# Performance work log

Measured on AMD Instinct MI355X. Metric: run time of the kernel, lower is better.

## Reference

```python
import jax, jax.numpy as jnp
import numpy as np

M = 12          # persons per frame
K = 2           # partition channels from conv1da (1024 = 2*512)
D = 512         # GCN channel dim / LSTM hidden
C_IN = 4096     # backbone feature dim
NUM_CLASSES = 8


def setup_inputs() -> dict:
    key = jax.random.key(0)
    ks = jax.random.split(key, 8)
    N, T = 16, 32
    NT = N * T
    base_out = jax.random.normal(ks[0], (NT, M, C_IN), dtype=jnp.float32)
    dist = jax.random.uniform(ks[1], (N, T, 3, K, M, M), dtype=jnp.float32)
    # conv1da: Conv1d(4096 -> 1024, k=1, bias=False) == matmul with [1024, 4096]
    w_a = jax.random.normal(ks[2], (K * D, C_IN), dtype=jnp.float32) * 0.02
    # LSTM(512, 512, 1): torch gate order i, f, g, o
    s = 1.0 / np.sqrt(D)
    w_ih = jax.random.uniform(ks[3], (4 * D, D), minval=-s, maxval=s, dtype=jnp.float32)
    w_hh = jax.random.uniform(ks[4], (4 * D, D), minval=-s, maxval=s, dtype=jnp.float32)
    b_ih = jax.random.uniform(ks[5], (4 * D,), minval=-s, maxval=s, dtype=jnp.float32)
    b_hh = jax.random.uniform(ks[6], (4 * D,), minval=-s, maxval=s, dtype=jnp.float32)
    # gclassifier: Linear(512 -> num_classes)
    w_cls = jax.random.normal(ks[7], (NUM_CLASSES, D), dtype=jnp.float32) * 0.01
    b_cls = jnp.zeros((NUM_CLASSES,), dtype=jnp.float32)
    return {"base_out": base_out, "dist": dist, "w_a": w_a,
            "w_ih": w_ih, "w_hh": w_hh, "b_ih": b_ih, "b_hh": b_hh,
            "w_cls": w_cls, "b_cls": b_cls, "n_videos": N}


def reference(base_out, dist, w_a, w_ih, w_hh, b_ih, b_hh, w_cls, b_cls, n_videos):
    NT = base_out.shape[0]
    N = n_videos
    T = NT // N
    # conv1da (1x1 conv, no bias): [NT, M, 4096] -> [NT, K*D, M] -> [NT, K, D, M]
    node1 = jnp.einsum('nmc,oc->nom', base_out, w_a).reshape(NT, K, D, M)
    # fused three-way adjacency aggregation: node1a + node1b + node1c
    A = (dist[:, :, 2] + dist[:, :, 1] + dist[:, :, 0]).reshape(NT, K, M, M)
    node = jnp.einsum('nkcv,nkvw->ncw', node1, A)  # [NT, D, M]
    node = jax.nn.relu(node)
    # AdaptiveAvgPool1d(1) over the M persons
    pooled = node.mean(axis=2)                      # [NT, D]
    seq = pooled.reshape(N, T, D)
    # torch nn.LSTM default batch_first=False: iterates over axis 0 (N), batch=T
    def step(carry, x_t):
        h, c = carry
        g = x_t @ w_ih.T + b_ih + h @ w_hh.T + b_hh  # [T, 4D]
        i, f, gg, o = jnp.split(g, 4, axis=-1)
        c = jax.nn.sigmoid(f) * c + jax.nn.sigmoid(i) * jnp.tanh(gg)
        h = jax.nn.sigmoid(o) * jnp.tanh(c)
        return (h, c), h
    h0 = jnp.zeros((T, D), dtype=seq.dtype)
    c0 = jnp.zeros((T, D), dtype=seq.dtype)
    _, hs = jax.lax.scan(step, (h0, c0), seq)       # [N, T, D]
    last = hs[:, -1, :]                              # video_feat[:, -1, :]
    return last @ w_cls.T + b_cls                    # [N, num_classes]
```

## Files before the change

### kernel.cpp

```cpp
#include <hip/hip_runtime.h>
#include <math.h>

#define MM 12
#define KK 2
#define DD 512
#define CIN 4096
#define NCLS 8
#define NV 16
#define TT 32

typedef unsigned long long u64;
typedef __attribute__((ext_vector_type(8))) __bf16 bf16x8;
typedef __attribute__((ext_vector_type(4))) float f32x4;

#define PART_F   0
#define POOLED_F 786432
#define TAGA_F   794624
#define TAGB_F   794880
#define PART_KS_STRIDE (192 * 1024)

#define MFMA_BF16(A, B, C) __builtin_amdgcn_mfma_f32_16x16x32_bf16((A), (B), (C), 0, 0, 0)

__global__ __launch_bounds__(256, 1) void k_fused(
    const float* __restrict__ base_out, const float* __restrict__ dist,
    const float* __restrict__ w_a, const float* __restrict__ w_ih,
    const float* __restrict__ w_hh, const float* __restrict__ b_ih,
    const float* __restrict__ b_hh, const float* __restrict__ w_cls,
    const float* __restrict__ b_cls,
    float* __restrict__ part, float* __restrict__ pooled,
    unsigned* __restrict__ tagA, unsigned* __restrict__ tagB,
    u64* __restrict__ slots, float* __restrict__ out)
{
  const int wg = blockIdx.x;
  const int tid = threadIdx.x;

  __shared__ __align__(16) unsigned short Ah[16 * 40], Al[16 * 40];
  __shared__ __align__(16) unsigned short Bh[192 * 40], Bl[192 * 40];
  __shared__ __align__(16) float whh_s[16][516];
  __shared__ __align__(16) float wih_s[16][516];
  __shared__ __align__(16) float pooled_s[16][520];
  __shared__ float gx_s[16][20];
  __shared__ __align__(16) float h_s[DD];
  __shared__ float dot_s[16];
  __shared__ float Asum_s[KK * MM * MM];

  {
    const int ks = wg >> 6, ot = wg & 63;
    const int cc0 = ks * 1024;
    const int wave = tid >> 6, lane = tid & 63;
    const int jf0 = wave * 3;

    const int sq = tid & 7;
    const int sr = tid >> 3;
    unsigned boff[6];
#pragma unroll
    for (int rep = 0; rep < 6; ++rep) {
      const int j = sr + 32 * rep;
      const int n = j / 12, m = j - n * 12;
      boff[rep] = (unsigned)(((n * TT + 31) * MM + m) * CIN + cc0 + sq * 4);
    }
    const bool aact = tid < 128;
    unsigned aoff = aact ? (unsigned)((ot * 16 + (tid >> 3)) * CIN + cc0 + sq * 4) : 0u;

    f32x4 acc0 = {0.f, 0.f, 0.f, 0.f}, acc1 = acc0, acc2 = acc0;

    float4 pa, pb[6];
    if (aact) pa = *(const float4*)&w_a[aoff];
#pragma unroll
    for (int rep = 0; rep < 6; ++rep) pb[rep] = *(const float4*)&base_out[boff[rep]];

    for (int st = 0; st < 32; ++st) {
      __syncthreads();
      if (aact) {
        const int idx = (tid >> 3) * 40 + sq * 4;
        unsigned ux = __float_as_uint(pa.x), uy = __float_as_uint(pa.y);
        unsigned uz = __float_as_uint(pa.z), uw = __float_as_uint(pa.w);
        *(uint2*)&Ah[idx] = make_uint2((ux >> 16) | (uy & 0xFFFF0000u),
                                       (uz >> 16) | (uw & 0xFFFF0000u));
        unsigned lx = __float_as_uint(pa.x - __uint_as_float(ux & 0xFFFF0000u));
        unsigned ly = __float_as_uint(pa.y - __uint_as_float(uy & 0xFFFF0000u));
        unsigned lz = __float_as_uint(pa.z - __uint_as_float(uz & 0xFFFF0000u));
        unsigned lw = __float_as_uint(pa.w - __uint_as_float(uw & 0xFFFF0000u));
        *(uint2*)&Al[idx] = make_uint2((lx >> 16) | (ly & 0xFFFF0000u),
                                       (lz >> 16) | (lw & 0xFFFF0000u));
      }
#pragma unroll
      for (int rep = 0; rep < 6; ++rep) {
        const int idx = (sr + 32 * rep) * 40 + sq * 4;
        unsigned ux = __float_as_uint(pb[rep].x), uy = __float_as_uint(pb[rep].y);
        unsigned uz = __float_as_uint(pb[rep].z), uw = __float_as_uint(pb[rep].w);
        *(uint2*)&Bh[idx] = make_uint2((ux >> 16) | (uy & 0xFFFF0000u),
                                       (uz >> 16) | (uw & 0xFFFF0000u));
        unsigned lx = __float_as_uint(pb[rep].x - __uint_as_float(ux & 0xFFFF0000u));
        unsigned ly = __float_as_uint(pb[rep].y - __uint_as_float(uy & 0xFFFF0000u));
        unsigned lz = __float_as_uint(pb[rep].z - __uint_as_float(uz & 0xFFFF0000u));
        unsigned lw = __float_as_uint(pb[rep].w - __uint_as_float(uw & 0xFFFF0000u));
        *(uint2*)&Bl[idx] = make_uint2((lx >> 16) | (ly & 0xFFFF0000u),
                                       (lz >> 16) | (lw & 0xFFFF0000u));
      }
      __syncthreads();
      if (st < 31) {
        aoff += 32;
        if (aact) pa = *(const float4*)&w_a[aoff];
#pragma unroll
        for (int rep = 0; rep < 6; ++rep) {
          boff[rep] += 32;
          pb[rep] = *(const float4*)&base_out[boff[rep]];
        }
      }
      const int koff = (lane >> 4) * 8;
      const int fra = (lane & 15) * 40 + koff;
      bf16x8 oh = *(const bf16x8*)&Ah[fra];
      bf16x8 ol = *(const bf16x8*)&Al[fra];
      {
        const int r0 = ((jf0 + 0) * 16 + (lane & 15)) * 40 + koff;
        bf16x8 jh = *(const bf16x8*)&Bh[r0], jl = *(const bf16x8*)&Bl[r0];
        acc0 = MFMA_BF16(jh, oh, acc0);
        acc0 = MFMA_BF16(jh, ol, acc0);
        acc0 = MFMA_BF16(jl, oh, acc0);
      }
      {
        const int r1 = ((jf0 + 1) * 16 + (lane & 15)) * 40 + koff;
        bf16x8 jh = *(const bf16x8*)&Bh[r1], jl = *(const bf16x8*)&Bl[r1];
        acc1 = MFMA_BF16(jh, oh, acc1);
        acc1 = MFMA_BF16(jh, ol, acc1);
        acc1 = MFMA_BF16(jl, oh, acc1);
      }
      {
        const int r2 = ((jf0 + 2) * 16 + (lane & 15)) * 40 + koff;
        bf16x8 jh = *(const bf16x8*)&Bh[r2], jl = *(const bf16x8*)&Bl[r2];
        acc2 = MFMA_BF16(jh, oh, acc2);
        acc2 = MFMA_BF16(jh, ol, acc2);
        acc2 = MFMA_BF16(jl, oh, acc2);
      }
    }
    const int o = ot * 16 + (lane & 15);
    const int jr = (lane >> 4) * 4;
#pragma unroll
    for (int r = 0; r < 4; ++r) {
      part[((size_t)ks * 192 + (jf0 + 0) * 16 + jr + r) * 1024 + o] = acc0[r];
      part[((size_t)ks * 192 + (jf0 + 1) * 16 + jr + r) * 1024 + o] = acc1[r];
      part[((size_t)ks * 192 + (jf0 + 2) * 16 + jr + r) * 1024 + o] = acc2[r];
    }
    __syncthreads();
    if (tid == 0)
      __hip_atomic_store(&tagA[wg], 1u, __ATOMIC_RELEASE, __HIP_MEMORY_SCOPE_AGENT);
  }

  if (wg < 128) {
    for (int f = tid; f < 16 * DD; f += 256) {
      const int rl = f >> 9, col = f & 511;
      const int row = (rl >> 2) * DD + wg * 4 + (rl & 3);
      whh_s[rl][col] = w_hh[(size_t)row * DD + col];
      wih_s[rl][col] = w_ih[(size_t)row * DD + col];
    }
  }

  while (__hip_atomic_load(&tagA[tid], __ATOMIC_RELAXED, __HIP_MEMORY_SCOPE_AGENT) != 1u) {}
  __syncthreads();
  (void)__hip_atomic_load(&tagA[0], __ATOMIC_ACQUIRE, __HIP_MEMORY_SCOPE_AGENT);

  {
    const int n = wg >> 4, cb = (wg & 15) * 32;
    const unsigned dbase = (unsigned)((n * TT + 31) * (3 * KK * MM * MM));
    for (int f = tid; f < KK * MM * MM; f += 256)
      Asum_s[f] = dist[dbase + f] + dist[dbase + KK * MM * MM + f]
                + dist[dbase + 2 * KK * MM * MM + f];
    __syncthreads();
    if (tid < 32) {
      const int c = cb + tid;
      float nd[KK][MM];
#pragma unroll
      for (int k = 0; k < KK; ++k)
#pragma unroll
        for (int v = 0; v < MM; ++v) {
          const size_t off = (size_t)(n * MM + v) * 1024 + k * DD + c;
          nd[k][v] = part[off] + part[off + PART_KS_STRIDE]
                   + part[off + 2 * PART_KS_STRIDE] + part[off + 3 * PART_KS_STRIDE];
        }
      float accm = 0.f;
#pragma unroll
      for (int w = 0; w < MM; ++w) {
        float sw = 0.f;
#pragma unroll
        for (int k = 0; k < KK; ++k)
#pragma unroll
          for (int v = 0; v < MM; ++v) sw += nd[k][v] * Asum_s[(k * MM + v) * MM + w];
        accm += fmaxf(sw, 0.f);
      }
      pooled[n * DD + c] = accm * (1.f / 12.f);
    }
    __syncthreads();
    if (tid == 0)
      __hip_atomic_store(&tagB[wg], 1u, __ATOMIC_RELEASE, __HIP_MEMORY_SCOPE_AGENT);
  }
  if (wg >= 128) return;

  while (__hip_atomic_load(&tagB[tid], __ATOMIC_RELAXED, __HIP_MEMORY_SCOPE_AGENT) != 1u) {}
  __syncthreads();
  (void)__hip_atomic_load(&tagB[0], __ATOMIC_ACQUIRE, __HIP_MEMORY_SCOPE_AGENT);

  for (int f = tid; f < NV * DD; f += 256) pooled_s[f >> 9][f & 511] = pooled[f];
  __syncthreads();
  {
    const int rl = tid & 15, n = tid >> 4;
    const float4* wr = (const float4*)&wih_s[rl][0];
    const float4* pv = (const float4*)&pooled_s[n][0];
    float a = 0.f;
#pragma unroll 8
    for (int q = 0; q < DD / 4; ++q) {
      float4 x = wr[q], y = pv[q];
      a += x.x * y.x + x.y * y.y + x.z * y.z + x.w * y.w;
    }
    const int row = (rl >> 2) * DD + wg * 4 + (rl & 3);
    gx_s[n][rl] = a + b_ih[row] + b_hh[row];
  }
  __syncthreads();

  {
    float c_reg = 0.f;
    const int r = tid >> 4;
    const int lj = tid & 15;

    for (int s = 0; s < NV; ++s) {
      if (s == 0) {
        h_s[tid] = 0.f; h_s[tid + 256] = 0.f;
      } else {
        const u64* slot = slots + ((size_t)(wg & 7) * NV + (s - 1)) * DD;
        u64 v0 = __hip_atomic_load(&slot[tid], __ATOMIC_RELAXED, __HIP_MEMORY_SCOPE_AGENT);
        u64 v1 = __hip_atomic_load(&slot[tid + 256], __ATOMIC_RELAXED, __HIP_MEMORY_SCOPE_AGENT);
        while ((unsigned)v0 != (unsigned)s)
          v0 = __hip_atomic_load(&slot[tid], __ATOMIC_RELAXED, __HIP_MEMORY_SCOPE_AGENT);
        while ((unsigned)v1 != (unsigned)s)
          v1 = __hip_atomic_load(&slot[tid + 256], __ATOMIC_RELAXED, __HIP_MEMORY_SCOPE_AGENT);
        h_s[tid] = __uint_as_float((unsigned)(v0 >> 32));
        h_s[tid + 256] = __uint_as_float((unsigned)(v1 >> 32));
      }
      __syncthreads();

      float p = 0.f;
      const float4* wrow = (const float4*)&whh_s[r][0];
      const float4* hv4 = (const float4*)h_s;
#pragma unroll
      for (int q = 0; q < 8; ++q) {
        float4 wv = wrow[lj + 16 * q];
        float4 hv = hv4[lj + 16 * q];
        p += wv.x * hv.x + wv.y * hv.y + wv.z * hv.z + wv.w * hv.w;
      }
#pragma unroll
      for (int off = 8; off; off >>= 1) p += __shfl_down(p, off, 16);
      if (lj == 0) dot_s[r] = p;
      __syncthreads();

      u64 pack = 0;
      if (tid < 4) {
        const float pi = gx_s[s][tid]      + dot_s[tid];
        const float pf = gx_s[s][4 + tid]  + dot_s[4 + tid];
        const float pg = gx_s[s][8 + tid]  + dot_s[8 + tid];
        const float po = gx_s[s][12 + tid] + dot_s[12 + tid];
        const float si = 1.f / (1.f + expf(-pi));
        const float sf = 1.f / (1.f + expf(-pf));
        const float so = 1.f / (1.f + expf(-po));
        c_reg = sf * c_reg + si * tanhf(pg);
        const float hn = so * tanhf(c_reg);
        pack = ((u64)__float_as_uint(hn) << 32) | (u64)(unsigned)(s + 1);
      }
      if (tid < 32) {
        u64 pk = __shfl(pack, tid & 3, 64);
        const int rep = tid >> 2;
        __hip_atomic_store(&slots[((size_t)rep * NV + s) * DD + wg * 4 + (tid & 3)], pk,
                           __ATOMIC_RELAXED, __HIP_MEMORY_SCOPE_AGENT);
      }
    }
  }

  if (wg == 0) {
    __syncthreads();
    for (int f = tid; f < NV * DD; f += 256) {
      const int ss = f >> 9, d = f & 511;
      u64 v = __hip_atomic_load(&slots[(size_t)ss * DD + d],
                                __ATOMIC_RELAXED, __HIP_MEMORY_SCOPE_AGENT);
      while ((unsigned)v != (unsigned)(ss + 1))
        v = __hip_atomic_load(&slots[(size_t)ss * DD + d],
                              __ATOMIC_RELAXED, __HIP_MEMORY_SCOPE_AGENT);
      pooled_s[ss][d] = __uint_as_float((unsigned)(v >> 32));
    }
    __syncthreads();
    if (tid < NV * NCLS) {
      const int n = tid >> 3, cl = tid & 7;
      const float4* hv = (const float4*)&pooled_s[n][0];
      const float4* wv = (const float4*)(w_cls + (size_t)cl * DD);
      float a = b_cls[cl];
#pragma unroll 8
      for (int q = 0; q < DD / 4; ++q) {
        float4 x = hv[q], y = wv[q];
        a += x.x * y.x + x.y * y.y + x.z * y.z + x.w * y.w;
      }
      out[tid] = a;
    }
  }
}

extern "C" void kernel_launch(void* const* d_in, const int* in_sizes, int n_in,
                              void* d_out, int out_size, void* d_ws, size_t ws_size,
                              hipStream_t stream) {
  const float* base_out = (const float*)d_in[0];
  const float* dist     = (const float*)d_in[1];
  const float* w_a      = (const float*)d_in[2];
  const float* w_ih     = (const float*)d_in[3];
  const float* w_hh     = (const float*)d_in[4];
  const float* b_ih     = (const float*)d_in[5];
  const float* b_hh     = (const float*)d_in[6];
  const float* w_cls    = (const float*)d_in[7];
  const float* b_cls    = (const float*)d_in[8];
  float* out = (float*)d_out;

  float* ws = (float*)d_ws;
  float* part   = ws + PART_F;
  float* pooled = ws + POOLED_F;
  unsigned* tagA = (unsigned*)(ws + TAGA_F);
  unsigned* tagB = (unsigned*)(ws + TAGB_F);
  u64* slots = (u64*)ws;

  k_fused<<<dim3(256), 256, 0, stream>>>(base_out, dist, w_a, w_ih, w_hh,
                                         b_ih, b_hh, w_cls, b_cls,
                                         part, pooled, tagA, tagB, slots, out);
}
```

Measured before the change: 273.2 us.

## Split fused persistent kernel into four launches and shrink LSTM grid

Breaks the single persistent kernel with global tag spin-barriers into separate GEMM, pooling, LSTM and classifier launches, relying on stream ordering instead of inter-block flag polling. The LSTM stage now runs on 32 workgroups of 512 threads, each owning 16 hidden units, with W_hh rows held in registers. Fewer blocks take part in the per-step slot exchange. This trades three extra kernel launch gaps for cheaper global barriers and less per-step communication fan-in. The recurrent slot buffer is moved to a separate workspace region when the workspace is large enough.

```diff
diff --git a/kernel.cpp b/kernel.cpp
--- a/kernel.cpp
+++ b/kernel.cpp
@@ -15,289 +15,272 @@
 
 #define PART_F   0
 #define POOLED_F 786432
-#define TAGA_F   794624
-#define TAGB_F   794880
+#define SLOTC_F  795136
+#define SLOTC_END_BYTES ((size_t)(795136 + 65536) * 4)
 #define PART_KS_STRIDE (192 * 1024)
 
 #define MFMA_BF16(A, B, C) __builtin_amdgcn_mfma_f32_16x16x32_bf16((A), (B), (C), 0, 0, 0)
 
-__global__ __launch_bounds__(256, 1) void k_fused(
-    const float* __restrict__ base_out, const float* __restrict__ dist,
-    const float* __restrict__ w_a, const float* __restrict__ w_ih,
-    const float* __restrict__ w_hh, const float* __restrict__ b_ih,
-    const float* __restrict__ b_hh, const float* __restrict__ w_cls,
-    const float* __restrict__ b_cls,
-    float* __restrict__ part, float* __restrict__ pooled,
-    unsigned* __restrict__ tagA, unsigned* __restrict__ tagB,
-    u64* __restrict__ slots, float* __restrict__ out)
-{
+__global__ __launch_bounds__(256, 1) void k_gemm(const float* __restrict__ w_a,
+                                                 const float* __restrict__ base_out,
+                                                 float* __restrict__ part) {
   const int wg = blockIdx.x;
   const int tid = threadIdx.x;
 
   __shared__ __align__(16) unsigned short Ah[16 * 40], Al[16 * 40];
   __shared__ __align__(16) unsigned short Bh[192 * 40], Bl[192 * 40];
-  __shared__ __align__(16) float whh_s[16][516];
-  __shared__ __align__(16) float wih_s[16][516];
-  __shared__ __align__(16) float pooled_s[16][520];
-  __shared__ float gx_s[16][20];
+
+  const int ks = wg >> 6, ot = wg & 63;
+  const int cc0 = ks * 1024;
+  const int wave = tid >> 6, lane = tid & 63;
+  const int jf0 = wave * 3;
+
+  const int sq = tid & 7;
+  const int sr = tid >> 3;
+  unsigned boff[6];
+#pragma unroll
+  for (int rep = 0; rep < 6; ++rep) {
+    const int j = sr + 32 * rep;
+    const int n = j / 12, m = j - n * 12;
+    boff[rep] = (unsigned)(((n * TT + 31) * MM + m) * CIN + cc0 + sq * 4);
+  }
+  const bool aact = tid < 128;
+  unsigned aoff = aact ? (unsigned)((ot * 16 + (tid >> 3)) * CIN + cc0 + sq * 4) : 0u;
+
+  f32x4 acc0 = {0.f, 0.f, 0.f, 0.f}, acc1 = acc0, acc2 = acc0;
+
+  float4 pa, pb[6];
+  if (aact) pa = *(const float4*)&w_a[aoff];
+#pragma unroll
+  for (int rep = 0; rep < 6; ++rep) pb[rep] = *(const float4*)&base_out[boff[rep]];
+
+  for (int st = 0; st < 32; ++st) {
+    __syncthreads();
+    if (aact) {
+      const int idx = (tid >> 3) * 40 + sq * 4;
+      unsigned ux = __float_as_uint(pa.x), uy = __float_as_uint(pa.y);
+      unsigned uz = __float_as_uint(pa.z), uw = __float_as_uint(pa.w);
+      *(uint2*)&Ah[idx] = make_uint2((ux >> 16) | (uy & 0xFFFF0000u),
+                                     (uz >> 16) | (uw & 0xFFFF0000u));
+      unsigned lx = __float_as_uint(pa.x - __uint_as_float(ux & 0xFFFF0000u));
+      unsigned ly = __float_as_uint(pa.y - __uint_as_float(uy & 0xFFFF0000u));
+      unsigned lz = __float_as_uint(pa.z - __uint_as_float(uz & 0xFFFF0000u));
+      unsigned lw = __float_as_uint(pa.w - __uint_as_float(uw & 0xFFFF0000u));
+      *(uint2*)&Al[idx] = make_uint2((lx >> 16) | (ly & 0xFFFF0000u),
+                                     (lz >> 16) | (lw & 0xFFFF0000u));
+    }
+#pragma unroll
+    for (int rep = 0; rep < 6; ++rep) {
+      const int idx = (sr + 32 * rep) * 40 + sq * 4;
+      unsigned ux = __float_as_uint(pb[rep].x), uy = __float_as_uint(pb[rep].y);
+      unsigned uz = __float_as_uint(pb[rep].z), uw = __float_as_uint(pb[rep].w);
+      *(uint2*)&Bh[idx] = make_uint2((ux >> 16) | (uy & 0xFFFF0000u),
+                                     (uz >> 16) | (uw & 0xFFFF0000u));
+      unsigned lx = __float_as_uint(pb[rep].x - __uint_as_float(ux & 0xFFFF0000u));
+      unsigned ly = __float_as_uint(pb[rep].y - __uint_as_float(uy & 0xFFFF0000u));
+      unsigned lz = __float_as_uint(pb[rep].z - __uint_as_float(uz & 0xFFFF0000u));
+      unsigned lw = __float_as_uint(pb[rep].w - __uint_as_float(uw & 0xFFFF0000u));
+      *(uint2*)&Bl[idx] = make_uint2((lx >> 16) | (ly & 0xFFFF0000u),
+                                     (lz >> 16) | (lw & 0xFFFF0000u));
+    }
+    __syncthreads();
+    if (st < 31) {
+      aoff += 32;
+      if (aact) pa = *(const float4*)&w_a[aoff];
+#pragma unroll
+      for (int rep = 0; rep < 6; ++rep) {
+        boff[rep] += 32;
+        pb[rep] = *(const float4*)&base_out[boff[rep]];
+      }
+    }
+    const int koff = (lane >> 4) * 8;
+    const int fra = (lane & 15) * 40 + koff;
+    bf16x8 oh = *(const bf16x8*)&Ah[fra];
+    bf16x8 ol = *(const bf16x8*)&Al[fra];
+    {
+      const int r0 = ((jf0 + 0) * 16 + (lane & 15)) * 40 + koff;
+      bf16x8 jh = *(const bf16x8*)&Bh[r0], jl = *(const bf16x8*)&Bl[r0];
+      acc0 = MFMA_BF16(jh, oh, acc0);
+      acc0 = MFMA_BF16(jh, ol, acc0);
+      acc0 = MFMA_BF16(jl, oh, acc0);
+    }
+    {
+      const int r1 = ((jf0 + 1) * 16 + (lane & 15)) * 40 + koff;
+      bf16x8 jh = *(const bf16x8*)&Bh[r1], jl = *(const bf16x8*)&Bl[r1];
+      acc1 = MFMA_BF16(jh, oh, acc1);
+      acc1 = MFMA_BF16(jh, ol, acc1);
+      acc1 = MFMA_BF16(jl, oh, acc1);
+    }
+    {
+      const int r2 = ((jf0 + 2) * 16 + (lane & 15)) * 40 + koff;
+      bf16x8 jh = *(const bf16x8*)&Bh[r2], jl = *(const bf16x8*)&Bl[r2];
+      acc2 = MFMA_BF16(jh, oh, acc2);
+      acc2 = MFMA_BF16(jh, ol, acc2);
+      acc2 = MFMA_BF16(jl, oh, acc2);
+    }
+  }
+  const int o = ot * 16 + (lane & 15);
+  const int jr = (lane >> 4) * 4;
+#pragma unroll
+  for (int r = 0; r < 4; ++r) {
+    part[((size_t)ks * 192 + (jf0 + 0) * 16 + jr + r) * 1024 + o] = acc0[r];
+    part[((size_t)ks * 192 + (jf0 + 1) * 16 + jr + r) * 1024 + o] = acc1[r];
+    part[((size_t)ks * 192 + (jf0 + 2) * 16 + jr + r) * 1024 + o] = acc2[r];
+  }
+}
+
+__global__ __launch_bounds__(256) void k_pool(const float* __restrict__ part,
+                                              const float* __restrict__ dist,
+                                              float* __restrict__ pooled) {
+  const int wg = blockIdx.x;
+  const int tid = threadIdx.x;
+  __shared__ float Asum_s[KK * MM * MM];
+  const int n = wg >> 4, cb = (wg & 15) * 32;
+  const unsigned dbase = (unsigned)((n * TT + 31) * (3 * KK * MM * MM));
+  for (int f = tid; f < KK * MM * MM; f += 256)
+    Asum_s[f] = dist[dbase + f] + dist[dbase + KK * MM * MM + f]
+              + dist[dbase + 2 * KK * MM * MM + f];
+  __syncthreads();
+  if (tid < 32) {
+    const int c = cb + tid;
+    float nd[KK][MM];
+#pragma unroll
+    for (int k = 0; k < KK; ++k)
+#pragma unroll
+      for (int v = 0; v < MM; ++v) {
+        const size_t off = (size_t)(n * MM + v) * 1024 + k * DD + c;
+        nd[k][v] = part[off] + part[off + PART_KS_STRIDE]
+                 + part[off + 2 * PART_KS_STRIDE] + part[off + 3 * PART_KS_STRIDE];
+      }
+    float accm = 0.f;
+#pragma unroll
+    for (int w = 0; w < MM; ++w) {
+      float sw = 0.f;
+#pragma unroll
+      for (int k = 0; k < KK; ++k)
+#pragma unroll
+        for (int v = 0; v < MM; ++v) sw += nd[k][v] * Asum_s[(k * MM + v) * MM + w];
+      accm += fmaxf(sw, 0.f);
+    }
+    pooled[n * DD + c] = accm * (1.f / 12.f);
+  }
+}
+
+__global__ __launch_bounds__(512, 1) void k_lstm(const float* __restrict__ w_hh,
+                                                 const float* __restrict__ w_ih,
+                                                 const float* __restrict__ b_ih,
+                                                 const float* __restrict__ b_hh,
+                                                 const float* __restrict__ pooled,
+                                                 u64* __restrict__ slots) {
+  const int wg = blockIdx.x;
+  const int tid = threadIdx.x;
+  const int r = tid >> 3;
+  const int l = tid & 7;
+  const int grow = (r >> 4) * DD + wg * 16 + (r & 15);
+
+  __shared__ __align__(16) float wih_s[64][516];
   __shared__ __align__(16) float h_s[DD];
-  __shared__ float dot_s[16];
-  __shared__ float Asum_s[KK * MM * MM];
-
-  {
-    const int ks = wg >> 6, ot = wg & 63;
-    const int cc0 = ks * 1024;
-    const int wave = tid >> 6, lane = tid & 63;
-    const int jf0 = wave * 3;
-
-    const int sq = tid & 7;
-    const int sr = tid >> 3;
-    unsigned boff[6];
-#pragma unroll
-    for (int rep = 0; rep < 6; ++rep) {
-      const int j = sr + 32 * rep;
-      const int n = j / 12, m = j - n * 12;
-      boff[rep] = (unsigned)(((n * TT + 31) * MM + m) * CIN + cc0 + sq * 4);
-    }
-    const bool aact = tid < 128;
-    unsigned aoff = aact ? (unsigned)((ot * 16 + (tid >> 3)) * CIN + cc0 + sq * 4) : 0u;
-
-    f32x4 acc0 = {0.f, 0.f, 0.f, 0.f}, acc1 = acc0, acc2 = acc0;
-
-    float4 pa, pb[6];
-    if (aact) pa = *(const float4*)&w_a[aoff];
-#pragma unroll
-    for (int rep = 0; rep < 6; ++rep) pb[rep] = *(const float4*)&base_out[boff[rep]];
-
-    for (int st = 0; st < 32; ++st) {
-      __syncthreads();
-      if (aact) {
-        const int idx = (tid >> 3) * 40 + sq * 4;
-        unsigned ux = __float_as_uint(pa.x), uy = __float_as_uint(pa.y);
-        unsigned uz = __float_as_uint(pa.z), uw = __float_as_uint(pa.w);
-        *(uint2*)&Ah[idx] = make_uint2((ux >> 16) | (uy & 0xFFFF0000u),
-                                       (uz >> 16) | (uw & 0xFFFF0000u));
-        unsigned lx = __float_as_uint(pa.x - __uint_as_float(ux & 0xFFFF0000u));
-        unsigned ly = __float_as_uint(pa.y - __uint_as_float(uy & 0xFFFF0000u));
-        unsigned lz = __float_as_uint(pa.z - __uint_as_float(uz & 0xFFFF0000u));
-        unsigned lw = __float_as_uint(pa.w - __uint_as_float(uw & 0xFFFF0000u));
-        *(uint2*)&Al[idx] = make_uint2((lx >> 16) | (ly & 0xFFFF0000u),
-                                       (lz >> 16) | (lw & 0xFFFF0000u));
-      }
-#pragma unroll
-      for (int rep = 0; rep < 6; ++rep) {
-        const int idx = (sr + 32 * rep) * 40 + sq * 4;
-        unsigned ux = __float_as_uint(pb[rep].x), uy = __float_as_uint(pb[rep].y);
-        unsigned uz = __float_as_uint(pb[rep].z), uw = __float_as_uint(pb[rep].w);
-        *(uint2*)&Bh[idx] = make_uint2((ux >> 16) | (uy & 0xFFFF0000u),
-                                       (uz >> 16) | (uw & 0xFFFF0000u));
-        unsigned lx = __float_as_uint(pb[rep].x - __uint_as_float(ux & 0xFFFF0000u));
-        unsigned ly = __float_as_uint(pb[rep].y - __uint_as_float(uy & 0xFFFF0000u));
-        unsigned lz = __float_as_uint(pb[rep].z - __uint_as_float(uz & 0xFFFF0000u));
-        unsigned lw = __float_as_uint(pb[rep].w - __uint_as_float(uw & 0xFFFF0000u));
-        *(uint2*)&Bl[idx] = make_uint2((lx >> 16) | (ly & 0xFFFF0000u),
-                                       (lz >> 16) | (lw & 0xFFFF0000u));
-      }
-      __syncthreads();
-      if (st < 31) {
-        aoff += 32;
-        if (aact) pa = *(const float4*)&w_a[aoff];
-#pragma unroll
-        for (int rep = 0; rep < 6; ++rep) {
-          boff[rep] += 32;
-          pb[rep] = *(const float4*)&base_out[boff[rep]];
-        }
-      }
-      const int koff = (lane >> 4) * 8;
-      const int fra = (lane & 15) * 40 + koff;
-      bf16x8 oh = *(const bf16x8*)&Ah[fra];
-      bf16x8 ol = *(const bf16x8*)&Al[fra];
-      {
-        const int r0 = ((jf0 + 0) * 16 + (lane & 15)) * 40 + koff;
-        bf16x8 jh = *(const bf16x8*)&Bh[r0], jl = *(const bf16x8*)&Bl[r0];
-        acc0 = MFMA_BF16(jh, oh, acc0);
-        acc0 = MFMA_BF16(jh, ol, acc0);
-        acc0 = MFMA_BF16(jl, oh, acc0);
-      }
-      {
-        const int r1 = ((jf0 + 1) * 16 + (lane & 15)) * 40 + koff;
-        bf16x8 jh = *(const bf16x8*)&Bh[r1], jl = *(const bf16x8*)&Bl[r1];
-        acc1 = MFMA_BF16(jh, oh, acc1);
-        acc1 = MFMA_BF16(jh, ol, acc1);
-        acc1 = MFMA_BF16(jl, oh, acc1);
-      }
-      {
-        const int r2 = ((jf0 + 2) * 16 + (lane & 15)) * 40 + koff;
-        bf16x8 jh = *(const bf16x8*)&Bh[r2], jl = *(const bf16x8*)&Bl[r2];
-        acc2 = MFMA_BF16(jh, oh, acc2);
-        acc2 = MFMA_BF16(jh, ol, acc2);
-        acc2 = MFMA_BF16(jl, oh, acc2);
-      }
-    }
-    const int o = ot * 16 + (lane & 15);
-    const int jr = (lane >> 4) * 4;
-#pragma unroll
-    for (int r = 0; r < 4; ++r) {
-      part[((size_t)ks * 192 + (jf0 + 0) * 16 + jr + r) * 1024 + o] = acc0[r];
-      part[((size_t)ks * 192 + (jf0 + 1) * 16 + jr + r) * 1024 + o] = acc1[r];
-      part[((size_t)ks * 192 + (jf0 + 2) * 16 + jr + r) * 1024 + o] = acc2[r];
-    }
-    __syncthreads();
-    if (tid == 0)
-      __hip_atomic_store(&tagA[wg], 1u, __ATOMIC_RELEASE, __HIP_MEMORY_SCOPE_AGENT);
-  }
-
-  if (wg < 128) {
-    for (int f = tid; f < 16 * DD; f += 256) {
-      const int rl = f >> 9, col = f & 511;
-      const int row = (rl >> 2) * DD + wg * 4 + (rl & 3);
-      whh_s[rl][col] = w_hh[(size_t)row * DD + col];
-      wih_s[rl][col] = w_ih[(size_t)row * DD + col];
-    }
-  }
-
-  while (__hip_atomic_load(&tagA[tid], __ATOMIC_RELAXED, __HIP_MEMORY_SCOPE_AGENT) != 1u) {}
+  __shared__ float dot_s[64];
+  __shared__ float gx_s[16][64];
+
+  float4 wr[16];
+#pragma unroll
+  for (int q = 0; q < 16; ++q)
+    wr[q] = *(const float4*)&w_hh[(size_t)grow * DD + l * 64 + q * 4];
+
+  for (int it = 0; it < 64; ++it) {
+    const int rg = (it >> 4) * DD + wg * 16 + (it & 15);
+    wih_s[it][tid] = w_ih[(size_t)rg * DD + tid];
+  }
   __syncthreads();
-  (void)__hip_atomic_load(&tagA[0], __ATOMIC_ACQUIRE, __HIP_MEMORY_SCOPE_AGENT);
-
-  {
-    const int n = wg >> 4, cb = (wg & 15) * 32;
-    const unsigned dbase = (unsigned)((n * TT + 31) * (3 * KK * MM * MM));
-    for (int f = tid; f < KK * MM * MM; f += 256)
-      Asum_s[f] = dist[dbase + f] + dist[dbase + KK * MM * MM + f]
-                + dist[dbase + 2 * KK * MM * MM + f];
-    __syncthreads();
-    if (tid < 32) {
-      const int c = cb + tid;
-      float nd[KK][MM];
-#pragma unroll
-      for (int k = 0; k < KK; ++k)
-#pragma unroll
-        for (int v = 0; v < MM; ++v) {
-          const size_t off = (size_t)(n * MM + v) * 1024 + k * DD + c;
-          nd[k][v] = part[off] + part[off + PART_KS_STRIDE]
-                   + part[off + 2 * PART_KS_STRIDE] + part[off + 3 * PART_KS_STRIDE];
-        }
-      float accm = 0.f;
-#pragma unroll
-      for (int w = 0; w < MM; ++w) {
-        float sw = 0.f;
-#pragma unroll
-        for (int k = 0; k < KK; ++k)
-#pragma unroll
-          for (int v = 0; v < MM; ++v) sw += nd[k][v] * Asum_s[(k * MM + v) * MM + w];
-        accm += fmaxf(sw, 0.f);
-      }
-      pooled[n * DD + c] = accm * (1.f / 12.f);
-    }
-    __syncthreads();
-    if (tid == 0)
-      __hip_atomic_store(&tagB[wg], 1u, __ATOMIC_RELEASE, __HIP_MEMORY_SCOPE_AGENT);
-  }
-  if (wg >= 128) return;
-
-  while (__hip_atomic_load(&tagB[tid], __ATOMIC_RELAXED, __HIP_MEMORY_SCOPE_AGENT) != 1u) {}
-  __syncthreads();
-  (void)__hip_atomic_load(&tagB[0], __ATOMIC_ACQUIRE, __HIP_MEMORY_SCOPE_AGENT);
-
-  for (int f = tid; f < NV * DD; f += 256) pooled_s[f >> 9][f & 511] = pooled[f];
-  __syncthreads();
-  {
-    const int rl = tid & 15, n = tid >> 4;
-    const float4* wr = (const float4*)&wih_s[rl][0];
-    const float4* pv = (const float4*)&pooled_s[n][0];
+
+  for (int idx = tid; idx < 1024; idx += 512) {
+    const int rr = idx >> 4, n = idx & 15;
+    const float4* wv = (const float4*)&wih_s[rr][0];
+    const float4* pv = (const float4*)&pooled[n * DD];
     float a = 0.f;
 #pragma unroll 8
     for (int q = 0; q < DD / 4; ++q) {
-      float4 x = wr[q], y = pv[q];
+      float4 x = wv[q], y = pv[q];
       a += x.x * y.x + x.y * y.y + x.z * y.z + x.w * y.w;
     }
-    const int row = (rl >> 2) * DD + wg * 4 + (rl & 3);
-    gx_s[n][rl] = a + b_ih[row] + b_hh[row];
+    const int rg = (rr >> 4) * DD + wg * 16 + (rr & 15);
+    gx_s[n][rr] = a + b_ih[rg] + b_hh[rg];
   }
   __syncthreads();
 
-  {
-    float c_reg = 0.f;
-    const int r = tid >> 4;
-    const int lj = tid & 15;
-
-    for (int s = 0; s < NV; ++s) {
-      if (s == 0) {
-        h_s[tid] = 0.f; h_s[tid + 256] = 0.f;
-      } else {
-        const u64* slot = slots + ((size_t)(wg & 7) * NV + (s - 1)) * DD;
-        u64 v0 = __hip_atomic_load(&slot[tid], __ATOMIC_RELAXED, __HIP_MEMORY_SCOPE_AGENT);
-        u64 v1 = __hip_atomic_load(&slot[tid + 256], __ATOMIC_RELAXED, __HIP_MEMORY_SCOPE_AGENT);
-        while ((unsigned)v0 != (unsigned)s)
-          v0 = __hip_atomic_load(&slot[tid], __ATOMIC_RELAXED, __HIP_MEMORY_SCOPE_AGENT);
-        while ((unsigned)v1 != (unsigned)s)
-          v1 = __hip_atomic_load(&slot[tid + 256], __ATOMIC_RELAXED, __HIP_MEMORY_SCOPE_AGENT);
-        h_s[tid] = __uint_as_float((unsigned)(v0 >> 32));
-        h_s[tid + 256] = __uint_as_float((unsigned)(v1 >> 32));
-      }
-      __syncthreads();
-
-      float p = 0.f;
-      const float4* wrow = (const float4*)&whh_s[r][0];
-      const float4* hv4 = (const float4*)h_s;
-#pragma unroll
-      for (int q = 0; q < 8; ++q) {
-        float4 wv = wrow[lj + 16 * q];
-        float4 hv = hv4[lj + 16 * q];
-        p += wv.x * hv.x + wv.y * hv.y + wv.z * hv.z + wv.w * hv.w;
-      }
-#pragma unroll
-      for (int off = 8; off; off >>= 1) p += __shfl_down(p, off, 16);
-      if (lj == 0) dot_s[r] = p;
-      __syncthreads();
-
-      u64 pack = 0;
-      if (tid < 4) {
-        const float pi = gx_s[s][tid]      + dot_s[tid];
-        const float pf = gx_s[s][4 + tid]  + dot_s[4 + tid];
-        const float pg = gx_s[s][8 + tid]  + dot_s[8 + tid];
-        const float po = gx_s[s][12 + tid] + dot_s[12 + tid];
-        const float si = 1.f / (1.f + expf(-pi));
-        const float sf = 1.f / (1.f + expf(-pf));
-        const float so = 1.f / (1.f + expf(-po));
-        c_reg = sf * c_reg + si * tanhf(pg);
-        const float hn = so * tanhf(c_reg);
-        pack = ((u64)__float_as_uint(hn) << 32) | (u64)(unsigned)(s + 1);
-      }
-      if (tid < 32) {
-        u64 pk = __shfl(pack, tid & 3, 64);
-        const int rep = tid >> 2;
-        __hip_atomic_store(&slots[((size_t)rep * NV + s) * DD + wg * 4 + (tid & 3)], pk,
-                           __ATOMIC_RELAXED, __HIP_MEMORY_SCOPE_AGENT);
-      }
-    }
-  }
-
-  if (wg == 0) {
+  float c_reg = 0.f;
+  const int rep = wg & 3;
+
+  for (int s = 0; s < NV; ++s) {
+    if (s == 0) {
+      h_s[tid] = 0.f;
+    } else {
+      const u64* slot = slots + ((size_t)rep * NV + (s - 1)) * DD;
+      u64 v = __hip_atomic_load(&slot[tid], __ATOMIC_RELAXED, __HIP_MEMORY_SCOPE_AGENT);
+      while ((unsigned)v != (unsigned)s)
+        v = __hip_atomic_load(&slot[tid], __ATOMIC_RELAXED, __HIP_MEMORY_SCOPE_AGENT);
+      h_s[tid] = __uint_as_float((unsigned)(v >> 32));
+    }
     __syncthreads();
-    for (int f = tid; f < NV * DD; f += 256) {
-      const int ss = f >> 9, d = f & 511;
-      u64 v = __hip_atomic_load(&slots[(size_t)ss * DD + d],
-                                __ATOMIC_RELAXED, __HIP_MEMORY_SCOPE_AGENT);
-      while ((unsigned)v != (unsigned)(ss + 1))
-        v = __hip_atomic_load(&slots[(size_t)ss * DD + d],
-                              __ATOMIC_RELAXED, __HIP_MEMORY_SCOPE_AGENT);
-      pooled_s[ss][d] = __uint_as_float((unsigned)(v >> 32));
-    }
+
+    float p = 0.f;
+    const float4* h4 = (const float4*)h_s;
+#pragma unroll
+    for (int q = 0; q < 16; ++q) {
+      const int qq = (q + 2 * l) & 15;
+      float4 hv = h4[l * 16 + qq];
+      p += wr[qq].x * hv.x + wr[qq].y * hv.y + wr[qq].z * hv.z + wr[qq].w * hv.w;
+    }
+    p += __shfl_down(p, 4, 8);
+    p += __shfl_down(p, 2, 8);
+    p += __shfl_down(p, 1, 8);
+    if (l == 0) dot_s[r] = p;
     __syncthreads();
-    if (tid < NV * NCLS) {
-      const int n = tid >> 3, cl = tid & 7;
-      const float4* hv = (const float4*)&pooled_s[n][0];
-      const float4* wv = (const float4*)(w_cls + (size_t)cl * DD);
-      float a = b_cls[cl];
+
+    u64 pack = 0;
+    if (tid < 16) {
+      const float pi = gx_s[s][tid]      + dot_s[tid];
+      const float pf = gx_s[s][16 + tid] + dot_s[16 + tid];
+      const float pg = gx_s[s][32 + tid] + dot_s[32 + tid];
+      const float po = gx_s[s][48 + tid] + dot_s[48 + tid];
+      const float si = 1.f / (1.f + expf(-pi));
+      const float sf = 1.f / (1.f + expf(-pf));
+      const float so = 1.f / (1.f + expf(-po));
+      c_reg = sf * c_reg + si * tanhf(pg);
+      const float hn = so * tanhf(c_reg);
+      pack = ((u64)__float_as_uint(hn) << 32) | (u64)(unsigned)(s + 1);
+    }
+    if (tid < 64) {
+      u64 pk = __shfl(pack, tid & 15, 64);
+      __hip_atomic_store(&slots[(((size_t)(tid >> 4)) * NV + s) * DD + wg * 16 + (tid & 15)],
+                         pk, __ATOMIC_RELAXED, __HIP_MEMORY_SCOPE_AGENT);
+    }
+  }
+}
+
+__global__ __launch_bounds__(256) void k_cls(const u64* __restrict__ slots,
+                                             const float* __restrict__ w_cls,
+                                             const float* __restrict__ b_cls,
+                                             float* __restrict__ out) {
+  const int tid = threadIdx.x;
+  __shared__ __align__(16) float h_hist[NV][520];
+  for (int f = tid; f < NV * DD; f += 256) {
+    const int ss = f >> 9, d = f & 511;
+    h_hist[ss][d] = __uint_as_float((unsigned)(slots[(size_t)ss * DD + d] >> 32));
+  }
+  __syncthreads();
+  if (tid < NV * NCLS) {
+    const int n = tid >> 3, cl = tid & 7;
+    const float4* hv = (const float4*)&h_hist[n][0];
+    const float4* wv = (const float4*)(w_cls + (size_t)cl * DD);
+    float a = b_cls[cl];
 #pragma unroll 8
-      for (int q = 0; q < DD / 4; ++q) {
-        float4 x = hv[q], y = wv[q];
-        a += x.x * y.x + x.y * y.y + x.z * y.z + x.w * y.w;
-      }
-      out[tid] = a;
-    }
+    for (int q = 0; q < DD / 4; ++q) {
+      float4 x = hv[q], y = wv[q];
+      a += x.x * y.x + x.y * y.y + x.z * y.z + x.w * y.w;
+    }
+    out[tid] = a;
   }
 }
 
@@ -318,11 +301,10 @@
   float* ws = (float*)d_ws;
   float* part   = ws + PART_F;
   float* pooled = ws + POOLED_F;
-  unsigned* tagA = (unsigned*)(ws + TAGA_F);
-  unsigned* tagB = (unsigned*)(ws + TAGB_F);
-  u64* slots = (u64*)ws;
-
-  k_fused<<<dim3(256), 256, 0, stream>>>(base_out, dist, w_a, w_ih, w_hh,
-                                         b_ih, b_hh, w_cls, b_cls,
-                                         part, pooled, tagA, tagB, slots, out);
-}
+  u64* slots = (ws_size >= SLOTC_END_BYTES) ? (u64*)(ws + SLOTC_F) : (u64*)ws;
+
+  k_gemm<<<dim3(256), 256, 0, stream>>>(w_a, base_out, part);
+  k_pool<<<dim3(256), 256, 0, stream>>>(part, dist, pooled);
+  k_lstm<<<dim3(32), 512, 0, stream>>>(w_hh, w_ih, b_ih, b_hh, pooled, slots);
+  k_cls<<<dim3(1), 256, 0, stream>>>(slots, w_cls, b_cls, out);
+}
```

New measurement: 417.6 us. 52.8% more time.
